# Optimization experiments

Hardware: AMD Instinct MI355X
Metric: run time of the kernel (lower is better)

Reference implementation:

```python
import jax, jax.numpy as jnp
import numpy as np

N = 200_000        # nodes
E = 2_000_000      # edges (before self loops)
D = 128            # emb_dim
L = 5              # num_layer
NUM_ATOM = 120     # num_atom_type
NUM_CHI = 3        # num_chirality_tag
NUM_BOND = 6       # num_bond_type
NUM_DIR = 3        # num_bond_direction
EPS = 1e-5


def setup_inputs() -> dict:
    key = jax.random.key(0)
    ks = jax.random.split(key, 12)
    s = 0.1
    return {
        "x": jax.random.randint(ks[0], (N, 2), 0, 3, dtype=jnp.int64) if jax.config.jax_enable_x64 else jax.random.randint(ks[0], (N, 2), 0, 3, dtype=jnp.int32),
        "edge_index": jax.random.randint(ks[1], (2, E), 0, N, dtype=jnp.int32),
        "edge_attr": jax.random.randint(ks[2], (E, 2), 0, 3, dtype=jnp.int32),
        "x_emb1": jax.random.normal(ks[3], (NUM_ATOM, D), jnp.float32) * s,
        "x_emb2": jax.random.normal(ks[4], (NUM_CHI, D), jnp.float32) * s,
        "edge_emb1": jax.random.normal(ks[5], (L, NUM_BOND, D), jnp.float32) * s,
        "edge_emb2": jax.random.normal(ks[6], (L, NUM_DIR, D), jnp.float32) * s,
        "w1": jax.random.normal(ks[7], (L, D, 2 * D), jnp.float32) * s,
        "b1": jnp.zeros((L, 2 * D), jnp.float32),
        "w2": jax.random.normal(ks[8], (L, 2 * D, D), jnp.float32) * s,
        "b2": jnp.zeros((L, D), jnp.float32),
        "bn_gamma": jnp.ones((L, D), jnp.float32),
        "bn_beta": jnp.zeros((L, D), jnp.float32),
    }


def reference(x, edge_index, edge_attr, x_emb1, x_emb2, edge_emb1, edge_emb2,
              w1, b1, w2, b2, bn_gamma, bn_beta):
    # node features: atom-type emb + chirality emb
    h = x_emb1[x[:, 0]] + x_emb2[x[:, 1]]                     # [N, D]

    # add self loops; self-loop edge_attr = [4, 0]
    loop = jnp.arange(N, dtype=edge_index.dtype)
    src = jnp.concatenate([edge_index[0], loop])              # [E+N]
    dst = jnp.concatenate([edge_index[1], loop])              # [E+N]
    ea0 = jnp.concatenate([edge_attr[:, 0], jnp.full((N,), 4, edge_attr.dtype)])
    ea1 = jnp.concatenate([edge_attr[:, 1], jnp.zeros((N,), edge_attr.dtype)])

    for l in range(L):
        e_emb = edge_emb1[l][ea0] + edge_emb2[l][ea1]         # [E+N, D]
        msg = h[src] + e_emb                                  # gather + add
        agg = jax.ops.segment_sum(msg, dst, num_segments=N)   # scatter-add
        hid = jax.nn.relu(agg @ w1[l] + b1[l])                # [N, 2D]
        hn = hid @ w2[l] + b2[l]                              # [N, D]
        # BatchNorm1d (training mode, biased variance)
        mean = hn.mean(axis=0)
        var = jnp.mean((hn - mean) ** 2, axis=0)
        hn = bn_gamma[l] * (hn - mean) * jax.lax.rsqrt(var + EPS) + bn_beta[l]
        if l < L - 1:
            hn = jax.nn.relu(hn)
        h = hn
    return h
```

## Files before the change

### kernel.cpp

```cpp
#include <hip/hip_runtime.h>

#define NN 200000
#define NPAD 200192
#define NE 2000000
#define DD 128
#define EPSF 1e-5f

typedef short short4v __attribute__((ext_vector_type(4)));
typedef short short8v __attribute__((ext_vector_type(8)));
typedef float f32x4 __attribute__((ext_vector_type(4)));
typedef unsigned long long u64;

__device__ __forceinline__ ushort f2bf(float f) {
  uint u = __float_as_uint(f);
  uint r = u + 0x7fff + ((u >> 16) & 1);
  return (ushort)(r >> 16);
}
__device__ __forceinline__ float bf2f(ushort u) { return __uint_as_float(((uint)u) << 16); }
__device__ __forceinline__ float bflo(uint v) { return __uint_as_float(v << 16); }
__device__ __forceinline__ float bfhi(uint v) { return __uint_as_float(v & 0xffff0000u); }
__device__ __forceinline__ uint packbf(float a, float b) {
  return (uint)f2bf(a) | ((uint)f2bf(b) << 16);
}

__device__ __forceinline__ short8v ldfrag(const ushort* p) {
  short4v lo = *(const short4v*)p;
  short4v hi = *(const short4v*)(p + 16);
  short8v r;
  r[0] = lo[0]; r[1] = lo[1]; r[2] = lo[2]; r[3] = lo[3];
  r[4] = hi[0]; r[5] = hi[1]; r[6] = hi[2]; r[7] = hi[3];
  return r;
}

__global__ __launch_bounds__(256) void k_init(const int* __restrict__ x,
    const float* __restrict__ e1, const float* __restrict__ e2,
    uint* __restrict__ h) {
  int t = blockIdx.x * 256 + threadIdx.x;
  if (t >= NN * 64) return;
  int node = t >> 6, cp = (t & 63) << 1;
  int a = x[2 * node], b = x[2 * node + 1];
  float2 va = *(const float2*)(e1 + (size_t)a * DD + cp);
  float2 vb = *(const float2*)(e2 + (size_t)b * DD + cp);
  h[t] = packbf(va.x + vb.x, va.y + vb.y);
}

__global__ __launch_bounds__(256) void k_cvtw(const float* __restrict__ w,
    ushort* __restrict__ wt, int K, int Nc) {
  int t = blockIdx.x * 256 + threadIdx.x;
  if (t >= 5 * K * Nc) return;
  int per = K * Nc;
  int l = t / per, r0 = t % per;
  int j = r0 & 7, lane = (r0 >> 3) & 63, idx = r0 >> 9;
  int KB = K >> 5;
  int kb = idx % KB, ct = idx / KB;
  int lr = lane & 15, qq = lane >> 4;
  int n = ct * 16 + lr;
  int k = kb * 32 + qq * 4 + (j & 3) + ((j >> 2) << 4);
  wt[t] = f2bf(w[(size_t)l * per + (size_t)k * Nc + n]);
}

__global__ __launch_bounds__(256) void k_hist(const int* __restrict__ ei,
    const int* __restrict__ ea, u64* __restrict__ hist8) {
  int e = blockIdx.x * 256 + threadIdx.x;
  if (e >= NE) return;
  int d = ei[NE + e];
  int a0 = ea[2 * e];
  int a1 = ea[2 * e + 1];
  u64 v = (1ull << (a0 * 10)) | (1ull << (30 + a1 * 10));
  atomicAdd(&hist8[(size_t)(blockIdx.x & 7) * NN + d], v);
}

__global__ __launch_bounds__(256) void k_scan1(const u64* __restrict__ hist8,
    u64* __restrict__ histsum, int* __restrict__ off, int* __restrict__ bsum) {
  __shared__ int sh[256];
  int i = blockIdx.x * 256 + threadIdx.x;
  int v = 0;
  if (i < NN) {
    u64 s = 0;
#pragma unroll
    for (int cc = 0; cc < 8; ++cc) s += hist8[(size_t)cc * NN + i];
    histsum[i] = s;
    v = (int)((s & 1023) + ((s >> 10) & 1023) + ((s >> 20) & 1023));
  }
  sh[threadIdx.x] = v;
  __syncthreads();
  for (int d = 1; d < 256; d <<= 1) {
    int xv = 0;
    if (threadIdx.x >= d) xv = sh[threadIdx.x - d];
    __syncthreads();
    if (threadIdx.x >= d) sh[threadIdx.x] += xv;
    __syncthreads();
  }
  if (i < NN) off[i] = sh[threadIdx.x] - v;
  if (threadIdx.x == 255) bsum[blockIdx.x] = sh[255];
}

__global__ __launch_bounds__(1024) void k_scan2(const int* __restrict__ bsum,
    int* __restrict__ boff, int nb) {
  __shared__ int sh[1024];
  int t = threadIdx.x;
  int v = (t < nb) ? bsum[t] : 0;
  sh[t] = v;
  __syncthreads();
  for (int d = 1; d < 1024; d <<= 1) {
    int xv = 0;
    if (t >= d) xv = sh[t - d];
    __syncthreads();
    if (t >= d) sh[t] += xv;
    __syncthreads();
  }
  if (t < nb) boff[t] = sh[t] - v;
}

__global__ __launch_bounds__(256) void k_scan3(int* __restrict__ off,
    const int* __restrict__ boff, const u64* __restrict__ hist8,
    int* __restrict__ cursor8) {
  int i = blockIdx.x * 256 + threadIdx.x;
  if (i < NN) {
    int o = off[i] + boff[i >> 8];
    off[i] = o;
    int run = o;
#pragma unroll
    for (int s = 0; s < 8; ++s) {
      cursor8[(size_t)s * NN + i] = run;
      u64 hs = hist8[(size_t)s * NN + i];
      run += (int)((hs & 1023) + ((hs >> 10) & 1023) + ((hs >> 20) & 1023));
    }
  }
  if (i == 0) off[NN] = NE;
}

__global__ __launch_bounds__(256) void k_scatter(const int* __restrict__ ei,
    int* __restrict__ cursor8, int* __restrict__ csr_src) {
  int e = blockIdx.x * 256 + threadIdx.x;
  if (e >= NE) return;
  int d = ei[NE + e];
  int p = atomicAdd(&cursor8[(size_t)(blockIdx.x & 7) * NN + d], 1);
  csr_src[p] = ei[e];
}

__global__ __launch_bounds__(256) void k_agg(const uint* __restrict__ h,
    uint* __restrict__ agghi, uint* __restrict__ agglo,
    const int* __restrict__ off, const int* __restrict__ src,
    const u64* __restrict__ hist,
    const float* __restrict__ E1, const float* __restrict__ E2) {
  int lane = threadIdx.x & 63;
  int node = blockIdx.x * 4 + (threadIdx.x >> 6);
  int qq = lane >> 4;
  int c = lane & 15;
  float a[8];
#pragma unroll
  for (int j = 0; j < 8; ++j) a[j] = 0.f;
  int beg = off[node], end = off[node + 1];
  int deg = end - beg;
  for (int base = 0; base < deg; base += 64) {
    int nrem = min(deg - base, 64);
    int myidx = 0;
    if (lane < nrem) myidx = src[beg + base + lane];
    int niter = (nrem + 3) >> 2;
    for (int m = 0; m < niter; m += 4) {
      int sl0 = qq + 4 * m;
      int sl1 = sl0 + 4, sl2 = sl0 + 8, sl3 = sl0 + 12;
      int s0 = __shfl(myidx, min(sl0, nrem - 1));
      int s1 = __shfl(myidx, min(sl1, nrem - 1));
      int s2 = __shfl(myidx, min(sl2, nrem - 1));
      int s3 = __shfl(myidx, min(sl3, nrem - 1));
      uint4 v0 = *(const uint4*)(h + (size_t)s0 * 64 + c * 4);
      if (sl0 < nrem) {
        a[0] += bflo(v0.x); a[1] += bfhi(v0.x);
        a[2] += bflo(v0.y); a[3] += bfhi(v0.y);
        a[4] += bflo(v0.z); a[5] += bfhi(v0.z);
        a[6] += bflo(v0.w); a[7] += bfhi(v0.w);
      }
      if (m + 1 < niter) {
        uint4 v1 = *(const uint4*)(h + (size_t)s1 * 64 + c * 4);
        if (sl1 < nrem) {
          a[0] += bflo(v1.x); a[1] += bfhi(v1.x);
          a[2] += bflo(v1.y); a[3] += bfhi(v1.y);
          a[4] += bflo(v1.z); a[5] += bfhi(v1.z);
          a[6] += bflo(v1.w); a[7] += bfhi(v1.w);
        }
      }
      if (m + 2 < niter) {
        uint4 v2 = *(const uint4*)(h + (size_t)s2 * 64 + c * 4);
        if (sl2 < nrem) {
          a[0] += bflo(v2.x); a[1] += bfhi(v2.x);
          a[2] += bflo(v2.y); a[3] += bfhi(v2.y);
          a[4] += bflo(v2.z); a[5] += bfhi(v2.z);
          a[6] += bflo(v2.w); a[7] += bfhi(v2.w);
        }
      }
      if (m + 3 < niter) {
        uint4 v3 = *(const uint4*)(h + (size_t)s3 * 64 + c * 4);
        if (sl3 < nrem) {
          a[0] += bflo(v3.x); a[1] += bfhi(v3.x);
          a[2] += bflo(v3.y); a[3] += bfhi(v3.y);
          a[4] += bflo(v3.z); a[5] += bfhi(v3.z);
          a[6] += bflo(v3.w); a[7] += bfhi(v3.w);
        }
      }
    }
  }
#pragma unroll
  for (int j = 0; j < 8; ++j) {
    a[j] += __shfl_xor(a[j], 16);
    a[j] += __shfl_xor(a[j], 32);
  }
  if (lane < 16) {
    uint4 sv = *(const uint4*)(h + (size_t)node * 64 + c * 4);
    a[0] += bflo(sv.x); a[1] += bfhi(sv.x);
    a[2] += bflo(sv.y); a[3] += bfhi(sv.y);
    a[4] += bflo(sv.z); a[5] += bfhi(sv.z);
    a[6] += bflo(sv.w); a[7] += bfhi(sv.w);
    u64 hv = hist[node];
    float cnt[7] = {
      (float)(int)(hv & 1023),
      (float)(int)((hv >> 10) & 1023),
      (float)(int)((hv >> 20) & 1023),
      1.f,
      (float)(int)((hv >> 30) & 1023) + 1.f,
      (float)(int)((hv >> 40) & 1023),
      (float)(int)((hv >> 50) & 1023)
    };
    const float* rows[7] = {E1, E1 + DD, E1 + 2 * DD, E1 + 4 * DD,
                            E2, E2 + DD, E2 + 2 * DD};
#pragma unroll
    for (int q = 0; q < 7; ++q) {
      f32x4 e0 = *(const f32x4*)(rows[q] + c * 8);
      f32x4 e1v = *(const f32x4*)(rows[q] + c * 8 + 4);
#pragma unroll
      for (int j = 0; j < 4; ++j) { a[j] += cnt[q] * e0[j]; a[4 + j] += cnt[q] * e1v[j]; }
    }
    uint4 hi4, lo4;
    {
      ushort hA, hB;
      hA = f2bf(a[0]); hB = f2bf(a[1]);
      hi4.x = (uint)hA | ((uint)hB << 16);
      lo4.x = (uint)f2bf(a[0] - bf2f(hA)) | ((uint)f2bf(a[1] - bf2f(hB)) << 16);
      hA = f2bf(a[2]); hB = f2bf(a[3]);
      hi4.y = (uint)hA | ((uint)hB << 16);
      lo4.y = (uint)f2bf(a[2] - bf2f(hA)) | ((uint)f2bf(a[3] - bf2f(hB)) << 16);
      hA = f2bf(a[4]); hB = f2bf(a[5]);
      hi4.z = (uint)hA | ((uint)hB << 16);
      lo4.z = (uint)f2bf(a[4] - bf2f(hA)) | ((uint)f2bf(a[5] - bf2f(hB)) << 16);
      hA = f2bf(a[6]); hB = f2bf(a[7]);
      hi4.w = (uint)hA | ((uint)hB << 16);
      lo4.w = (uint)f2bf(a[6] - bf2f(hA)) | ((uint)f2bf(a[7] - bf2f(hB)) << 16);
    }
    *(uint4*)(agghi + (size_t)node * 64 + c * 4) = hi4;
    *(uint4*)(agglo + (size_t)node * 64 + c * 4) = lo4;
  }
}

__global__ __launch_bounds__(512, 1) void k_mlp(
    const ushort* __restrict__ agghi, const ushort* __restrict__ agglo,
    const ushort* __restrict__ w1,
    const float* __restrict__ b1,
    const ushort* __restrict__ w2,
    const float* __restrict__ b2, uint* __restrict__ hnb,
    float* __restrict__ bnsums) {
  __shared__ uint4 smem4[8192];
  __shared__ float sstat[256];
  const ushort* sw1 = (const ushort*)smem4;
  const ushort* sw2 = (const ushort*)(smem4 + 4096);
  int t = threadIdx.x;
  int lane = t & 63;
  int wid = t >> 6;
  int nb = blockIdx.x * 256 + wid * 32;
  int lr = lane & 15, qq = lane >> 4;

  if (t < 256) sstat[t] = 0.f;

  short8v afh[2][4], afl[2][4];
#pragma unroll
  for (int g = 0; g < 2; ++g) {
    const ushort* ph = agghi + (size_t)(nb + g * 16 + lr) * 128 + qq * 4;
    const ushort* pl = agglo + (size_t)(nb + g * 16 + lr) * 128 + qq * 4;
#pragma unroll
    for (int kb = 0; kb < 4; ++kb) {
      afh[g][kb] = ldfrag(ph + kb * 32);
      afl[g][kb] = ldfrag(pl + kb * 32);
    }
  }

  {
    const uint4* g1 = (const uint4*)w1;
    const uint4* g2 = (const uint4*)w2;
#pragma unroll
    for (int i = 0; i < 8; ++i) smem4[i * 512 + t] = g1[i * 512 + t];
#pragma unroll
    for (int i = 0; i < 8; ++i) smem4[4096 + i * 512 + t] = g2[i * 512 + t];
  }
  __syncthreads();

  f32x4 acc2[2][8];
#pragma unroll
  for (int g = 0; g < 2; ++g)
#pragma unroll
    for (int ct = 0; ct < 8; ++ct) acc2[g][ct] = (f32x4){0.f, 0.f, 0.f, 0.f};

#pragma unroll
  for (int ph = 0; ph < 4; ++ph) {
    f32x4 acc1[2][4];
#pragma unroll
    for (int g = 0; g < 2; ++g)
#pragma unroll
      for (int ct = 0; ct < 4; ++ct) acc1[g][ct] = (f32x4){0.f, 0.f, 0.f, 0.f};
#pragma unroll
    for (int ct = 0; ct < 4; ++ct) {
      int gct = ph * 4 + ct;
#pragma unroll
      for (int kb = 0; kb < 4; ++kb) {
        short8v wf = *(const short8v*)(sw1 + ((gct * 4 + kb) * 64 + lane) * 8);
        acc1[0][ct] = __builtin_amdgcn_mfma_f32_16x16x32_bf16(wf, afh[0][kb], acc1[0][ct], 0, 0, 0);
        acc1[0][ct] = __builtin_amdgcn_mfma_f32_16x16x32_bf16(wf, afl[0][kb], acc1[0][ct], 0, 0, 0);
        acc1[1][ct] = __builtin_amdgcn_mfma_f32_16x16x32_bf16(wf, afh[1][kb], acc1[1][ct], 0, 0, 0);
        acc1[1][ct] = __builtin_amdgcn_mfma_f32_16x16x32_bf16(wf, afl[1][kb], acc1[1][ct], 0, 0, 0);
      }
    }
    short8v hfh[2][2], hfl[2][2];
#pragma unroll
    for (int i = 0; i < 2; ++i) {
      f32x4 ba = *(const f32x4*)(b1 + (ph * 4 + 2 * i) * 16 + qq * 4);
      f32x4 bb = *(const f32x4*)(b1 + (ph * 4 + 2 * i + 1) * 16 + qq * 4);
#pragma unroll
      for (int g = 0; g < 2; ++g) {
        short8v hh, hl;
#pragma unroll
        for (int r = 0; r < 4; ++r) {
          float va = fmaxf(acc1[g][2 * i][r] + ba[r], 0.f);
          float vb = fmaxf(acc1[g][2 * i + 1][r] + bb[r], 0.f);
          ushort ha = f2bf(va), hb = f2bf(vb);
          hh[r] = (short)ha; hh[4 + r] = (short)hb;
          hl[r] = (short)f2bf(va - bf2f(ha));
          hl[4 + r] = (short)f2bf(vb - bf2f(hb));
        }
        hfh[g][i] = hh; hfl[g][i] = hl;
      }
    }
#pragma unroll
    for (int ct = 0; ct < 8; ++ct) {
#pragma unroll
      for (int i = 0; i < 2; ++i) {
        int kb2 = ph * 2 + i;
        short8v wf = *(const short8v*)(sw2 + ((ct * 8 + kb2) * 64 + lane) * 8);
        acc2[0][ct] = __builtin_amdgcn_mfma_f32_16x16x32_bf16(wf, hfh[0][i], acc2[0][ct], 0, 0, 0);
        acc2[0][ct] = __builtin_amdgcn_mfma_f32_16x16x32_bf16(wf, hfl[0][i], acc2[0][ct], 0, 0, 0);
        acc2[1][ct] = __builtin_amdgcn_mfma_f32_16x16x32_bf16(wf, hfh[1][i], acc2[1][ct], 0, 0, 0);
        acc2[1][ct] = __builtin_amdgcn_mfma_f32_16x16x32_bf16(wf, hfl[1][i], acc2[1][ct], 0, 0, 0);
      }
    }
  }

  int n0 = nb + lr, n1 = nb + 16 + lr;
  float m0 = (n0 < NN) ? 1.f : 0.f;
  float m1 = (n1 < NN) ? 1.f : 0.f;
#pragma unroll
  for (int ct = 0; ct < 8; ++ct) {
    f32x4 bb = *(const f32x4*)(b2 + ct * 16 + qq * 4);
    f32x4 o0, o1;
#pragma unroll
    for (int r = 0; r < 4; ++r) {
      o0[r] = acc2[0][ct][r] + bb[r];
      o1[r] = acc2[1][ct][r] + bb[r];
    }
#pragma unroll
    for (int r = 0; r < 4; ++r) {
      float s = m0 * o0[r] + m1 * o1[r];
      float q = m0 * o0[r] * o0[r] + m1 * o1[r] * o1[r];
      s += __shfl_xor(s, 1); q += __shfl_xor(q, 1);
      s += __shfl_xor(s, 2); q += __shfl_xor(q, 2);
      s += __shfl_xor(s, 4); q += __shfl_xor(q, 4);
      s += __shfl_xor(s, 8); q += __shfl_xor(q, 8);
      if (lr == 0) {
        int col = ct * 16 + qq * 4 + r;
        atomicAdd(&sstat[col], s);
        atomicAdd(&sstat[128 + col], q);
      }
    }
    if (n0 < NN) {
      uint2 wv;
      wv.x = packbf(o0[0], o0[1]);
      wv.y = packbf(o0[2], o0[3]);
      *(uint2*)(hnb + (size_t)n0 * 64 + ct * 8 + qq * 2) = wv;
    }
    if (n1 < NN) {
      uint2 wv;
      wv.x = packbf(o1[0], o1[1]);
      wv.y = packbf(o1[2], o1[3]);
      *(uint2*)(hnb + (size_t)n1 * 64 + ct * 8 + qq * 2) = wv;
    }
  }
  __syncthreads();
  if (t < 256) atomicAdd(&bnsums[t], sstat[t]);
}

__global__ __launch_bounds__(256) void k_bnapply(const uint* __restrict__ hnb,
    const float* __restrict__ sums, const float* __restrict__ gamma,
    const float* __restrict__ beta, uint* __restrict__ hout,
    float* __restrict__ fout, int final_layer) {
  int t = blockIdx.x * 256 + threadIdx.x;
  if (t >= NN * 64) return;
  int node = t >> 6, cp = (t & 63) << 1;
  uint v = hnb[t];
  float r[2] = {bflo(v), bfhi(v)};
#pragma unroll
  for (int j = 0; j < 2; ++j) {
    int col = cp + j;
    float mean = sums[col] * (1.f / NN);
    float var = sums[128 + col] * (1.f / NN) - mean * mean;
    float scale = gamma[col] * rsqrtf(var + EPSF);
    r[j] = (r[j] - mean) * scale + beta[col];
  }
  if (final_layer) {
    *(float2*)(fout + (size_t)node * DD + cp) = make_float2(r[0], r[1]);
  } else {
    hout[t] = packbf(fmaxf(r[0], 0.f), fmaxf(r[1], 0.f));
  }
}

extern "C" void kernel_launch(void* const* d_in, const int* in_sizes, int n_in,
                              void* d_out, int out_size, void* d_ws, size_t ws_size,
                              hipStream_t stream) {
  const int* x    = (const int*)d_in[0];
  const int* ei   = (const int*)d_in[1];
  const int* ea   = (const int*)d_in[2];
  const float* xe1 = (const float*)d_in[3];
  const float* xe2 = (const float*)d_in[4];
  const float* ee1 = (const float*)d_in[5];
  const float* ee2 = (const float*)d_in[6];
  const float* w1  = (const float*)d_in[7];
  const float* b1  = (const float*)d_in[8];
  const float* w2  = (const float*)d_in[9];
  const float* b2  = (const float*)d_in[10];
  const float* gam = (const float*)d_in[11];
  const float* bet = (const float*)d_in[12];
  float* out = (float*)d_out;

  char* p = (char*)d_ws;
  auto alloc = [&](size_t bytes) {
    char* r = p;
    p += (bytes + 255) & ~(size_t)255;
    return r;
  };
  uint* h      = (uint*)alloc((size_t)NN * 64 * 4);
  uint* agghi  = (uint*)alloc((size_t)NPAD * 64 * 4);
  uint* agglo  = (uint*)alloc((size_t)NPAD * 64 * 4);
  uint* hnb    = (uint*)alloc((size_t)NPAD * 64 * 4);
  ushort* w1t  = (ushort*)alloc((size_t)5 * 128 * 256 * 2);
  ushort* w2t  = (ushort*)alloc((size_t)5 * 256 * 128 * 2);
  u64* hist8   = (u64*)alloc((size_t)8 * NN * 8);
  u64* histsum = (u64*)alloc((size_t)NN * 8);
  int* csroff  = (int*)alloc((size_t)(NN + 1) * 4);
  int* cursor8 = (int*)alloc((size_t)8 * NN * 4);
  int* csrsrc  = (int*)alloc((size_t)NE * 4);
  int* bsum    = (int*)alloc(4096);
  int* boff    = (int*)alloc(4096);
  float* bnsums = (float*)alloc(5 * 1024);

  const int nscan = (NN + 255) / 256;

  hipMemsetAsync(hist8, 0, (size_t)8 * NN * 8, stream);
  hipMemsetAsync(bnsums, 0, 5 * 1024, stream);

  k_cvtw<<<(5 * 128 * 256 + 255) / 256, 256, 0, stream>>>(w1, w1t, 128, 256);
  k_cvtw<<<(5 * 256 * 128 + 255) / 256, 256, 0, stream>>>(w2, w2t, 256, 128);
  k_init<<<(NN * 64 + 255) / 256, 256, 0, stream>>>(x, xe1, xe2, h);
  k_hist<<<(NE + 255) / 256, 256, 0, stream>>>(ei, ea, hist8);
  k_scan1<<<nscan, 256, 0, stream>>>(hist8, histsum, csroff, bsum);
  k_scan2<<<1, 1024, 0, stream>>>(bsum, boff, nscan);
  k_scan3<<<nscan, 256, 0, stream>>>(csroff, boff, hist8, cursor8);
  k_scatter<<<(NE + 255) / 256, 256, 0, stream>>>(ei, cursor8, csrsrc);

  for (int l = 0; l < 5; ++l) {
    k_agg<<<NN / 4, 256, 0, stream>>>(h, agghi, agglo, csroff, csrsrc, histsum,
                                      ee1 + (size_t)l * 6 * DD,
                                      ee2 + (size_t)l * 3 * DD);
    k_mlp<<<NPAD / 256, 512, 0, stream>>>((const ushort*)agghi, (const ushort*)agglo,
                                          w1t + (size_t)l * 128 * 256,
                                          b1 + (size_t)l * 256,
                                          w2t + (size_t)l * 256 * 128,
                                          b2 + (size_t)l * DD, hnb,
                                          bnsums + (size_t)l * 256);
    k_bnapply<<<(NN * 64 + 255) / 256, 256, 0, stream>>>(
        hnb, bnsums + (size_t)l * 256, gam + (size_t)l * DD, bet + (size_t)l * DD,
        h, out, l == 4 ? 1 : 0);
  }
}
```

Measured before the change: 1.692 ms.

## Persistent MLP blocks with fragment-ordered aggregation output layout

The aggregation kernel now writes its hi/lo bf16 outputs permuted into MFMA-fragment order, so the MLP kernel can load each A-fragment with a single 16-byte load instead of two 8-byte loads. The MLP kernel becomes persistent: 256 blocks loop over 782 node tiles, staging the weights into shared memory once per block instead of once per tile. This cuts the repeated weight staging, but the tail is uneven (some blocks do 4 tiles, others 3) and the grid now relies on 256 blocks covering the CUs well.

```diff
diff --git a/kernel.cpp b/kernel.cpp
--- a/kernel.cpp
+++ b/kernel.cpp
@@ -2,6 +2,7 @@
 
 #define NN 200000
 #define NPAD 200192
+#define NTILES 782
 #define NE 2000000
 #define DD 128
 #define EPSF 1e-5f
@@ -21,15 +22,6 @@
 __device__ __forceinline__ float bfhi(uint v) { return __uint_as_float(v & 0xffff0000u); }
 __device__ __forceinline__ uint packbf(float a, float b) {
   return (uint)f2bf(a) | ((uint)f2bf(b) << 16);
-}
-
-__device__ __forceinline__ short8v ldfrag(const ushort* p) {
-  short4v lo = *(const short4v*)p;
-  short4v hi = *(const short4v*)(p + 16);
-  short8v r;
-  r[0] = lo[0]; r[1] = lo[1]; r[2] = lo[2]; r[3] = lo[3];
-  r[4] = hi[0]; r[5] = hi[1]; r[6] = hi[2]; r[7] = hi[3];
-  return r;
 }
 
 __global__ __launch_bounds__(256) void k_init(const int* __restrict__ x,
@@ -231,24 +223,25 @@
 #pragma unroll
       for (int j = 0; j < 4; ++j) { a[j] += cnt[q] * e0[j]; a[4 + j] += cnt[q] * e1v[j]; }
     }
-    uint4 hi4, lo4;
-    {
-      ushort hA, hB;
-      hA = f2bf(a[0]); hB = f2bf(a[1]);
-      hi4.x = (uint)hA | ((uint)hB << 16);
-      lo4.x = (uint)f2bf(a[0] - bf2f(hA)) | ((uint)f2bf(a[1] - bf2f(hB)) << 16);
-      hA = f2bf(a[2]); hB = f2bf(a[3]);
-      hi4.y = (uint)hA | ((uint)hB << 16);
-      lo4.y = (uint)f2bf(a[2] - bf2f(hA)) | ((uint)f2bf(a[3] - bf2f(hB)) << 16);
-      hA = f2bf(a[4]); hB = f2bf(a[5]);
-      hi4.z = (uint)hA | ((uint)hB << 16);
-      lo4.z = (uint)f2bf(a[4] - bf2f(hA)) | ((uint)f2bf(a[5] - bf2f(hB)) << 16);
-      hA = f2bf(a[6]); hB = f2bf(a[7]);
-      hi4.w = (uint)hA | ((uint)hB << 16);
-      lo4.w = (uint)f2bf(a[6] - bf2f(hA)) | ((uint)f2bf(a[7] - bf2f(hB)) << 16);
-    }
-    *(uint4*)(agghi + (size_t)node * 64 + c * 4) = hi4;
-    *(uint4*)(agglo + (size_t)node * 64 + c * 4) = lo4;
+    int wb = ((c >> 2) << 4) + ((c & 1) << 3) + (((c >> 1) & 1) << 1);
+    ushort hA, hB;
+    uint2 w01, w23, l01, l23;
+    hA = f2bf(a[0]); hB = f2bf(a[1]);
+    w01.x = (uint)hA | ((uint)hB << 16);
+    l01.x = (uint)f2bf(a[0] - bf2f(hA)) | ((uint)f2bf(a[1] - bf2f(hB)) << 16);
+    hA = f2bf(a[2]); hB = f2bf(a[3]);
+    w01.y = (uint)hA | ((uint)hB << 16);
+    l01.y = (uint)f2bf(a[2] - bf2f(hA)) | ((uint)f2bf(a[3] - bf2f(hB)) << 16);
+    hA = f2bf(a[4]); hB = f2bf(a[5]);
+    w23.x = (uint)hA | ((uint)hB << 16);
+    l23.x = (uint)f2bf(a[4] - bf2f(hA)) | ((uint)f2bf(a[5] - bf2f(hB)) << 16);
+    hA = f2bf(a[6]); hB = f2bf(a[7]);
+    w23.y = (uint)hA | ((uint)hB << 16);
+    l23.y = (uint)f2bf(a[6] - bf2f(hA)) | ((uint)f2bf(a[7] - bf2f(hB)) << 16);
+    *(uint2*)(agghi + (size_t)node * 64 + wb) = w01;
+    *(uint2*)(agghi + (size_t)node * 64 + wb + 4) = w23;
+    *(uint2*)(agglo + (size_t)node * 64 + wb) = l01;
+    *(uint2*)(agglo + (size_t)node * 64 + wb + 4) = l23;
   }
 }
 
@@ -266,22 +259,9 @@
   int t = threadIdx.x;
   int lane = t & 63;
   int wid = t >> 6;
-  int nb = blockIdx.x * 256 + wid * 32;
   int lr = lane & 15, qq = lane >> 4;
 
   if (t < 256) sstat[t] = 0.f;
-
-  short8v afh[2][4], afl[2][4];
-#pragma unroll
-  for (int g = 0; g < 2; ++g) {
-    const ushort* ph = agghi + (size_t)(nb + g * 16 + lr) * 128 + qq * 4;
-    const ushort* pl = agglo + (size_t)(nb + g * 16 + lr) * 128 + qq * 4;
-#pragma unroll
-    for (int kb = 0; kb < 4; ++kb) {
-      afh[g][kb] = ldfrag(ph + kb * 32);
-      afl[g][kb] = ldfrag(pl + kb * 32);
-    }
-  }
 
   {
     const uint4* g1 = (const uint4*)w1;
@@ -293,102 +273,118 @@
   }
   __syncthreads();
 
-  f32x4 acc2[2][8];
-#pragma unroll
-  for (int g = 0; g < 2; ++g)
-#pragma unroll
-    for (int ct = 0; ct < 8; ++ct) acc2[g][ct] = (f32x4){0.f, 0.f, 0.f, 0.f};
-
-#pragma unroll
-  for (int ph = 0; ph < 4; ++ph) {
-    f32x4 acc1[2][4];
+  for (int tile = blockIdx.x; tile < NTILES; tile += 256) {
+    int nb = tile * 256 + wid * 32;
+
+    short8v afh[2][4], afl[2][4];
+#pragma unroll
+    for (int g = 0; g < 2; ++g) {
+      const ushort* ph = agghi + (size_t)(nb + g * 16 + lr) * 128 + qq * 8;
+      const ushort* pl = agglo + (size_t)(nb + g * 16 + lr) * 128 + qq * 8;
+#pragma unroll
+      for (int kb = 0; kb < 4; ++kb) {
+        afh[g][kb] = *(const short8v*)(ph + kb * 32);
+        afl[g][kb] = *(const short8v*)(pl + kb * 32);
+      }
+    }
+
+    f32x4 acc2[2][8];
 #pragma unroll
     for (int g = 0; g < 2; ++g)
 #pragma unroll
-      for (int ct = 0; ct < 4; ++ct) acc1[g][ct] = (f32x4){0.f, 0.f, 0.f, 0.f};
-#pragma unroll
-    for (int ct = 0; ct < 4; ++ct) {
-      int gct = ph * 4 + ct;
-#pragma unroll
-      for (int kb = 0; kb < 4; ++kb) {
-        short8v wf = *(const short8v*)(sw1 + ((gct * 4 + kb) * 64 + lane) * 8);
-        acc1[0][ct] = __builtin_amdgcn_mfma_f32_16x16x32_bf16(wf, afh[0][kb], acc1[0][ct], 0, 0, 0);
-        acc1[0][ct] = __builtin_amdgcn_mfma_f32_16x16x32_bf16(wf, afl[0][kb], acc1[0][ct], 0, 0, 0);
-        acc1[1][ct] = __builtin_amdgcn_mfma_f32_16x16x32_bf16(wf, afh[1][kb], acc1[1][ct], 0, 0, 0);
-        acc1[1][ct] = __builtin_amdgcn_mfma_f32_16x16x32_bf16(wf, afl[1][kb], acc1[1][ct], 0, 0, 0);
-      }
-    }
-    short8v hfh[2][2], hfl[2][2];
-#pragma unroll
-    for (int i = 0; i < 2; ++i) {
-      f32x4 ba = *(const f32x4*)(b1 + (ph * 4 + 2 * i) * 16 + qq * 4);
-      f32x4 bb = *(const f32x4*)(b1 + (ph * 4 + 2 * i + 1) * 16 + qq * 4);
-#pragma unroll
-      for (int g = 0; g < 2; ++g) {
-        short8v hh, hl;
-#pragma unroll
-        for (int r = 0; r < 4; ++r) {
-          float va = fmaxf(acc1[g][2 * i][r] + ba[r], 0.f);
-          float vb = fmaxf(acc1[g][2 * i + 1][r] + bb[r], 0.f);
-          ushort ha = f2bf(va), hb = f2bf(vb);
-          hh[r] = (short)ha; hh[4 + r] = (short)hb;
-          hl[r] = (short)f2bf(va - bf2f(ha));
-          hl[4 + r] = (short)f2bf(vb - bf2f(hb));
-        }
-        hfh[g][i] = hh; hfl[g][i] = hl;
-      }
-    }
+      for (int ct = 0; ct < 8; ++ct) acc2[g][ct] = (f32x4){0.f, 0.f, 0.f, 0.f};
+
+#pragma unroll
+    for (int ph = 0; ph < 4; ++ph) {
+      f32x4 acc1[2][4];
+#pragma unroll
+      for (int g = 0; g < 2; ++g)
+#pragma unroll
+        for (int ct = 0; ct < 4; ++ct) acc1[g][ct] = (f32x4){0.f, 0.f, 0.f, 0.f};
+#pragma unroll
+      for (int ct = 0; ct < 4; ++ct) {
+        int gct = ph * 4 + ct;
+#pragma unroll
+        for (int kb = 0; kb < 4; ++kb) {
+          short8v wf = *(const short8v*)(sw1 + ((gct * 4 + kb) * 64 + lane) * 8);
+          acc1[0][ct] = __builtin_amdgcn_mfma_f32_16x16x32_bf16(wf, afh[0][kb], acc1[0][ct], 0, 0, 0);
+          acc1[0][ct] = __builtin_amdgcn_mfma_f32_16x16x32_bf16(wf, afl[0][kb], acc1[0][ct], 0, 0, 0);
+          acc1[1][ct] = __builtin_amdgcn_mfma_f32_16x16x32_bf16(wf, afh[1][kb], acc1[1][ct], 0, 0, 0);
+          acc1[1][ct] = __builtin_amdgcn_mfma_f32_16x16x32_bf16(wf, afl[1][kb], acc1[1][ct], 0, 0, 0);
+        }
+      }
+      short8v hfh[2][2], hfl[2][2];
+#pragma unroll
+      for (int i = 0; i < 2; ++i) {
+        f32x4 ba = *(const f32x4*)(b1 + (ph * 4 + 2 * i) * 16 + qq * 4);
+        f32x4 bb = *(const f32x4*)(b1 + (ph * 4 + 2 * i + 1) * 16 + qq * 4);
+#pragma unroll
+        for (int g = 0; g < 2; ++g) {
+          short8v hh, hl;
+#pragma unroll
+          for (int r = 0; r < 4; ++r) {
+            float va = fmaxf(acc1[g][2 * i][r] + ba[r], 0.f);
+            float vb = fmaxf(acc1[g][2 * i + 1][r] + bb[r], 0.f);
+            ushort ha = f2bf(va), hb = f2bf(vb);
+            hh[r] = (short)ha; hh[4 + r] = (short)hb;
+            hl[r] = (short)f2bf(va - bf2f(ha));
+            hl[4 + r] = (short)f2bf(vb - bf2f(hb));
+          }
+          hfh[g][i] = hh; hfl[g][i] = hl;
+        }
+      }
+#pragma unroll
+      for (int ct = 0; ct < 8; ++ct) {
+#pragma unroll
+        for (int i = 0; i < 2; ++i) {
+          int kb2 = ph * 2 + i;
+          short8v wf = *(const short8v*)(sw2 + ((ct * 8 + kb2) * 64 + lane) * 8);
+          acc2[0][ct] = __builtin_amdgcn_mfma_f32_16x16x32_bf16(wf, hfh[0][i], acc2[0][ct], 0, 0, 0);
+          acc2[0][ct] = __builtin_amdgcn_mfma_f32_16x16x32_bf16(wf, hfl[0][i], acc2[0][ct], 0, 0, 0);
+          acc2[1][ct] = __builtin_amdgcn_mfma_f32_16x16x32_bf16(wf, hfh[1][i], acc2[1][ct], 0, 0, 0);
+          acc2[1][ct] = __builtin_amdgcn_mfma_f32_16x16x32_bf16(wf, hfl[1][i], acc2[1][ct], 0, 0, 0);
+        }
+      }
+    }
+
+    int n0 = nb + lr, n1 = nb + 16 + lr;
+    float m0 = (n0 < NN) ? 1.f : 0.f;
+    float m1 = (n1 < NN) ? 1.f : 0.f;
 #pragma unroll
     for (int ct = 0; ct < 8; ++ct) {
-#pragma unroll
-      for (int i = 0; i < 2; ++i) {
-        int kb2 = ph * 2 + i;
-        short8v wf = *(const short8v*)(sw2 + ((ct * 8 + kb2) * 64 + lane) * 8);
-        acc2[0][ct] = __builtin_amdgcn_mfma_f32_16x16x32_bf16(wf, hfh[0][i], acc2[0][ct], 0, 0, 0);
-        acc2[0][ct] = __builtin_amdgcn_mfma_f32_16x16x32_bf16(wf, hfl[0][i], acc2[0][ct], 0, 0, 0);
-        acc2[1][ct] = __builtin_amdgcn_mfma_f32_16x16x32_bf16(wf, hfh[1][i], acc2[1][ct], 0, 0, 0);
-        acc2[1][ct] = __builtin_amdgcn_mfma_f32_16x16x32_bf16(wf, hfl[1][i], acc2[1][ct], 0, 0, 0);
-      }
-    }
-  }
-
-  int n0 = nb + lr, n1 = nb + 16 + lr;
-  float m0 = (n0 < NN) ? 1.f : 0.f;
-  float m1 = (n1 < NN) ? 1.f : 0.f;
-#pragma unroll
-  for (int ct = 0; ct < 8; ++ct) {
-    f32x4 bb = *(const f32x4*)(b2 + ct * 16 + qq * 4);
-    f32x4 o0, o1;
-#pragma unroll
-    for (int r = 0; r < 4; ++r) {
-      o0[r] = acc2[0][ct][r] + bb[r];
-      o1[r] = acc2[1][ct][r] + bb[r];
-    }
-#pragma unroll
-    for (int r = 0; r < 4; ++r) {
-      float s = m0 * o0[r] + m1 * o1[r];
-      float q = m0 * o0[r] * o0[r] + m1 * o1[r] * o1[r];
-      s += __shfl_xor(s, 1); q += __shfl_xor(q, 1);
-      s += __shfl_xor(s, 2); q += __shfl_xor(q, 2);
-      s += __shfl_xor(s, 4); q += __shfl_xor(q, 4);
-      s += __shfl_xor(s, 8); q += __shfl_xor(q, 8);
-      if (lr == 0) {
-        int col = ct * 16 + qq * 4 + r;
-        atomicAdd(&sstat[col], s);
-        atomicAdd(&sstat[128 + col], q);
-      }
-    }
-    if (n0 < NN) {
-      uint2 wv;
-      wv.x = packbf(o0[0], o0[1]);
-      wv.y = packbf(o0[2], o0[3]);
-      *(uint2*)(hnb + (size_t)n0 * 64 + ct * 8 + qq * 2) = wv;
-    }
-    if (n1 < NN) {
-      uint2 wv;
-      wv.x = packbf(o1[0], o1[1]);
-      wv.y = packbf(o1[2], o1[3]);
-      *(uint2*)(hnb + (size_t)n1 * 64 + ct * 8 + qq * 2) = wv;
+      f32x4 bb = *(const f32x4*)(b2 + ct * 16 + qq * 4);
+      f32x4 o0, o1;
+#pragma unroll
+      for (int r = 0; r < 4; ++r) {
+        o0[r] = acc2[0][ct][r] + bb[r];
+        o1[r] = acc2[1][ct][r] + bb[r];
+      }
+#pragma unroll
+      for (int r = 0; r < 4; ++r) {
+        float s = m0 * o0[r] + m1 * o1[r];
+        float q = m0 * o0[r] * o0[r] + m1 * o1[r] * o1[r];
+        s += __shfl_xor(s, 1); q += __shfl_xor(q, 1);
+        s += __shfl_xor(s, 2); q += __shfl_xor(q, 2);
+        s += __shfl_xor(s, 4); q += __shfl_xor(q, 4);
+        s += __shfl_xor(s, 8); q += __shfl_xor(q, 8);
+        if (lr == 0) {
+          int col = ct * 16 + qq * 4 + r;
+          atomicAdd(&sstat[col], s);
+          atomicAdd(&sstat[128 + col], q);
+        }
+      }
+      if (n0 < NN) {
+        uint2 wv;
+        wv.x = packbf(o0[0], o0[1]);
+        wv.y = packbf(o0[2], o0[3]);
+        *(uint2*)(hnb + (size_t)n0 * 64 + ct * 8 + qq * 2) = wv;
+      }
+      if (n1 < NN) {
+        uint2 wv;
+        wv.x = packbf(o1[0], o1[1]);
+        wv.y = packbf(o1[2], o1[3]);
+        *(uint2*)(hnb + (size_t)n1 * 64 + ct * 8 + qq * 2) = wv;
+      }
     }
   }
   __syncthreads();
@@ -476,12 +472,12 @@
     k_agg<<<NN / 4, 256, 0, stream>>>(h, agghi, agglo, csroff, csrsrc, histsum,
                                       ee1 + (size_t)l * 6 * DD,
                                       ee2 + (size_t)l * 3 * DD);
-    k_mlp<<<NPAD / 256, 512, 0, stream>>>((const ushort*)agghi, (const ushort*)agglo,
-                                          w1t + (size_t)l * 128 * 256,
-                                          b1 + (size_t)l * 256,
-                                          w2t + (size_t)l * 256 * 128,
-                                          b2 + (size_t)l * DD, hnb,
-                                          bnsums + (size_t)l * 256);
+    k_mlp<<<256, 512, 0, stream>>>((const ushort*)agghi, (const ushort*)agglo,
+                                   w1t + (size_t)l * 128 * 256,
+                                   b1 + (size_t)l * 256,
+                                   w2t + (size_t)l * 256 * 128,
+                                   b2 + (size_t)l * DD, hnb,
+                                   bnsums + (size_t)l * 256);
     k_bnapply<<<(NN * 64 + 255) / 256, 256, 0, stream>>>(
         hnb, bnsums + (size_t)l * 256, gam + (size_t)l * DD, bet + (size_t)l * DD,
         h, out, l == 4 ? 1 : 0);
```

Result: slower. 3.000 ms (+77.2%).
